# Performance work log

Measured on AMD Instinct MI355X. Metric: run time of the kernel, lower is better.

The kernel has to match this reference:

```python
import jax, jax.numpy as jnp
import numpy as np

N_NODES = 50000
N_EDGES = 800000
D_IN = 64
D_OUT = 64
EDGE_DIM = 32
BN_EPS = 1e-5
GIN_EPS = 0.0


def setup_inputs() -> dict:
    key = jax.random.key(0)
    ks = jax.random.split(key, 8)
    x = jax.random.normal(ks[0], (N_NODES, D_IN), dtype=jnp.float32)
    edge_index = jax.random.randint(ks[1], (2, N_EDGES), 0, N_NODES, dtype=jnp.int64)
    edge_attr = jax.random.normal(ks[2], (N_EDGES, EDGE_DIM), dtype=jnp.float32)
    # learned params (scaled like kaiming-ish init)
    We = jax.random.normal(ks[3], (EDGE_DIM, D_IN), dtype=jnp.float32) / np.sqrt(EDGE_DIM)
    be = jnp.zeros((D_IN,), dtype=jnp.float32)
    W1 = jax.random.normal(ks[4], (D_IN, D_OUT), dtype=jnp.float32) / np.sqrt(D_IN)
    b1 = jnp.zeros((D_OUT,), dtype=jnp.float32)
    gamma = jnp.ones((D_OUT,), dtype=jnp.float32)
    beta = jnp.zeros((D_OUT,), dtype=jnp.float32)
    W2 = jax.random.normal(ks[5], (D_OUT, D_OUT), dtype=jnp.float32) / np.sqrt(D_OUT)
    b2 = jnp.zeros((D_OUT,), dtype=jnp.float32)
    return {"x": x, "edge_index": edge_index, "edge_attr": edge_attr,
            "We": We, "be": be, "W1": W1, "b1": b1,
            "gamma": gamma, "beta": beta, "W2": W2, "b2": b2}


def reference(x, edge_index, edge_attr, We, be, W1, b1, gamma, beta, W2, b2):
    src = edge_index[0]  # j (source), PyG default flow source_to_target
    dst = edge_index[1]  # i (target)
    # message: x_j + lin(edge_attr)
    msg = x[src] + (edge_attr @ We + be)              # [E, D_IN]
    # scatter-add aggregate into target nodes
    agg = jax.ops.segment_sum(msg, dst, num_segments=x.shape[0])  # [N, D_IN]
    # GIN residual
    out = agg + (1.0 + GIN_EPS) * x
    # MLP: Linear -> BatchNorm1d (training stats) -> ReLU -> Linear
    h = out @ W1 + b1
    mean = jnp.mean(h, axis=0)
    var = jnp.var(h, axis=0)
    h = (h - mean) * jax.lax.rsqrt(var + BN_EPS) * gamma + beta
    h = jax.nn.relu(h)
    return h @ W2 + b2
```

## Files before the change

kernel.cpp:

```cpp
#include <hip/hip_runtime.h>

#define N_NODES 50000
#define N_EDGES 800000
#define D 64
#define ED 32
#define BN_EPS 1e-5f

#define NBKT 250
#define NPB  200
#define NB_SC 500
#define EPB  1600
#define CAP  4096

#define WS_SUMS     0
#define WS_SUMSQ    64
#define WS_RESV     128
#define WS_ZERO_END 384
#define WS_OFF      384
#define WS_PACK     50388
#define WS_SRC2     (WS_PACK + 2 * NBKT * CAP)
#define WS_AGGEA    (WS_SRC2 + 2 * N_EDGES)
#define WS_PRE      (WS_AGGEA + N_NODES * ED)
#define WS_H        (WS_PRE + N_NODES * D)
#define WS_WC       (WS_H + N_NODES * D)
#define WS_BEC      (WS_WC + ED * D)

#define N_BLK ((N_NODES + 63) / 64)

__global__ __launch_bounds__(256) void foldw_kernel(
    const float* __restrict__ We, const float* __restrict__ W1,
    const float* __restrict__ be, float* __restrict__ wc, float* __restrict__ bec)
{
    const int idx = blockIdx.x * 256 + threadIdx.x;
    if (idx < ED * D) {
        const int j = idx >> 6, f = idx & 63;
        float a = 0.f;
        for (int k = 0; k < D; ++k) a += We[j * D + k] * W1[k * D + f];
        wc[idx] = a;
    }
    if (idx < D) {
        float a = 0.f;
        for (int k = 0; k < D; ++k) a += be[k] * W1[k * D + idx];
        bec[idx] = a;
    }
}

__global__ __launch_bounds__(256) void bin_scatter_kernel(
    const int* __restrict__ ei, int* __restrict__ resv, uint2* __restrict__ pack)
{
    __shared__ int hist[NBKT], seg[NBKT], lcur[NBKT];
    const int t = threadIdx.x;
    if (t < NBKT) { hist[t] = 0; lcur[t] = 0; }
    __syncthreads();
    const int e0 = blockIdx.x * EPB;
    for (int i = t; i < EPB; i += 256)
        atomicAdd(&hist[ei[N_EDGES + e0 + i] / NPB], 1);
    __syncthreads();
    if (t < NBKT) seg[t] = t * CAP + atomicAdd(&resv[t], hist[t]);
    __syncthreads();
    for (int i = t; i < EPB; i += 256) {
        const int e = e0 + i;
        const int s = ei[e];
        const int d = ei[N_EDGES + e];
        const int bkt = d / NPB;
        const int r = atomicAdd(&lcur[bkt], 1);
        pack[seg[bkt] + r] = make_uint2(((unsigned)d << 16) | (unsigned)s,
                                        (unsigned)e);
    }
}

__global__ __launch_bounds__(512) void bucket_place_kernel(
    const int* __restrict__ resv, const uint2* __restrict__ pack,
    int* __restrict__ off, int2* __restrict__ sorted)
{
    __shared__ int sA[256], sB[256];
    __shared__ int cnt[NPB], lcur[NPB];
    __shared__ int pA[256], pB[256];
    __shared__ int sBase, sNE;
    const int t = threadIdx.x;
    const int j = blockIdx.x;
    if (t < 256) sA[t] = (t < NBKT) ? resv[t] : 0;
    if (t < NPB) { cnt[t] = 0; lcur[t] = 0; }
    __syncthreads();
    int* cur = sA; int* nxt = sB;
    for (int o = 1; o < 256; o <<= 1) {
        if (t < 256) nxt[t] = cur[t] + (t >= o ? cur[t - o] : 0);
        __syncthreads();
        int* tmp = cur; cur = nxt; nxt = tmp;
    }
    if (t == 0) { sBase = (j == 0) ? 0 : cur[j - 1]; sNE = resv[j]; }
    __syncthreads();
    const int base = sBase, nE = sNE;
    const uint2* pp = pack + (size_t)j * CAP;

    for (int i = t; i < nE; i += 512)
        atomicAdd(&cnt[(int)(pp[i].x >> 16) - j * NPB], 1);
    __syncthreads();
    if (t < 256) pA[t] = (t < NPB) ? cnt[t] : 0;
    __syncthreads();
    int* c2 = pA; int* n2 = pB;
    for (int o = 1; o < 256; o <<= 1) {
        if (t < 256) n2[t] = c2[t] + (t >= o ? c2[t - o] : 0);
        __syncthreads();
        int* tmp = c2; c2 = n2; n2 = tmp;
    }
    if (t < NPB) {
        const int excl = (t == 0) ? 0 : c2[t - 1];
        n2[t] = excl;
        off[j * NPB + t] = base + excl;
    }
    if (j == NBKT - 1 && t == 0) off[N_NODES] = N_EDGES;
    __syncthreads();
    for (int i = t; i < nE; i += 512) {
        const uint2 w = pp[i];
        const int dl = (int)(w.x >> 16) - j * NPB;
        const int r = atomicAdd(&lcur[dl], 1);
        sorted[base + n2[dl] + r] = make_int2((int)w.y, (int)(w.x & 0xffffu));
    }
}

__global__ __launch_bounds__(256) void agg_kernel(
    const float* __restrict__ x, const float* __restrict__ ea,
    const int* __restrict__ off, const int2* __restrict__ sorted,
    float* __restrict__ pre, float* __restrict__ aggEA)
{
    const int f = threadIdx.x & 63;
    const int w = threadIdx.x >> 6;
    const int fe = f & 31;
    const bool lo = (f < 32);
    const int nwv = gridDim.x * 4;
    for (int node = blockIdx.x * 4 + w; node < N_NODES; node += nwv) {
        const int start = __builtin_amdgcn_readfirstlane(off[node]);
        const int n     = __builtin_amdgcn_readfirstlane(off[node + 1]) - start;
        const int2* sp = sorted + start;
        float s = x[(size_t)node * D + f];
        float ax = 0.f, ay = 0.f;
        int it = 0;
        if (n >= 8) {
            int2 c0 = sp[0], c1 = sp[1], c2 = sp[2], c3 = sp[3];
            int2 c4 = sp[4], c5 = sp[5], c6 = sp[6], c7 = sp[7];
            for (; it + 16 <= n; it += 8) {
                const int2 n0 = sp[it + 8],  n1 = sp[it + 9];
                const int2 n2 = sp[it + 10], n3 = sp[it + 11];
                const int2 n4 = sp[it + 12], n5 = sp[it + 13];
                const int2 n6 = sp[it + 14], n7 = sp[it + 15];
                s += x[(size_t)c0.y * D + f]; s += x[(size_t)c1.y * D + f];
                s += x[(size_t)c2.y * D + f]; s += x[(size_t)c3.y * D + f];
                s += x[(size_t)c4.y * D + f]; s += x[(size_t)c5.y * D + f];
                s += x[(size_t)c6.y * D + f]; s += x[(size_t)c7.y * D + f];
                ax += ea[(size_t)(lo ? c0.x : c1.x) * ED + fe];
                ax += ea[(size_t)(lo ? c2.x : c3.x) * ED + fe];
                ay += ea[(size_t)(lo ? c4.x : c5.x) * ED + fe];
                ay += ea[(size_t)(lo ? c6.x : c7.x) * ED + fe];
                c0 = n0; c1 = n1; c2 = n2; c3 = n3;
                c4 = n4; c5 = n5; c6 = n6; c7 = n7;
            }
            s += x[(size_t)c0.y * D + f]; s += x[(size_t)c1.y * D + f];
            s += x[(size_t)c2.y * D + f]; s += x[(size_t)c3.y * D + f];
            s += x[(size_t)c4.y * D + f]; s += x[(size_t)c5.y * D + f];
            s += x[(size_t)c6.y * D + f]; s += x[(size_t)c7.y * D + f];
            ax += ea[(size_t)(lo ? c0.x : c1.x) * ED + fe];
            ax += ea[(size_t)(lo ? c2.x : c3.x) * ED + fe];
            ay += ea[(size_t)(lo ? c4.x : c5.x) * ED + fe];
            ay += ea[(size_t)(lo ? c6.x : c7.x) * ED + fe];
            it += 8;
        }
        for (; it < n; ++it) {
            const int2 p = sp[it];
            s += x[(size_t)p.y * D + f];
            if (lo) ax += ea[(size_t)p.x * ED + fe];
        }
        pre[(size_t)node * D + f] = s;
        ax += ay;
        ax += __shfl_xor(ax, 32);
        if (lo) aggEA[(size_t)node * ED + fe] = ax;
    }
}

__global__ __launch_bounds__(256) void mlp1g_kernel(
    const float* __restrict__ pre, const float* __restrict__ aggEA,
    const int* __restrict__ off,
    const float* __restrict__ W1, const float* __restrict__ wc,
    const float* __restrict__ bec, const float* __restrict__ b1,
    float* __restrict__ h, float* __restrict__ sums, float* __restrict__ sumsq)
{
    __shared__ float As[64 * 100];
    __shared__ float Bs[96 * 64];
    __shared__ float4 sb1v[16];
    __shared__ float4 sbecv[16];
    __shared__ float sDeg[64];
    const int tid = threadIdx.x;
    const int base = blockIdx.x * 64;

    for (int i = tid; i < 64 * 16; i += 256)
        ((float4*)Bs)[i] = ((const float4*)W1)[i];
    for (int i = tid; i < 32 * 16; i += 256)
        ((float4*)Bs)[64 * 16 + i] = ((const float4*)wc)[i];
    if (tid < 16)      sb1v[tid] = ((const float4*)b1)[tid];
    else if (tid < 32) sbecv[tid - 16] = ((const float4*)bec)[tid - 16];
    if (tid < 64) {
        const int node = base + tid;
        sDeg[tid] = (node < N_NODES) ? (float)(off[node + 1] - off[node]) : 0.f;
    }
    #pragma unroll
    for (int r = 0; r < 4; ++r) {
        const int idx = tid + 256 * r;
        const int nl = idx >> 4, c4 = idx & 15;
        const bool v = (base + nl) < N_NODES;
        const float4 t = v ? ((const float4*)pre)[(size_t)(base + nl) * 16 + c4]
                           : make_float4(0.f, 0.f, 0.f, 0.f);
        *(float4*)&As[nl * 100 + c4 * 4] = t;
    }
    #pragma unroll
    for (int r = 0; r < 2; ++r) {
        const int idx = tid + 256 * r;
        const int nl = idx >> 3, c4 = idx & 7;
        const bool v = (base + nl) < N_NODES;
        const float4 t = v ? ((const float4*)aggEA)[(size_t)(base + nl) * 8 + c4]
                           : make_float4(0.f, 0.f, 0.f, 0.f);
        *(float4*)&As[nl * 100 + 64 + c4 * 4] = t;
    }
    __syncthreads();

    const int tx = tid & 15, ty = tid >> 4;
    const int r0 = ty * 4;
    const float4 bb = sb1v[tx];
    const float4 bc = sbecv[tx];
    float4 acc0, acc1, acc2, acc3;
    acc0.x = bb.x + sDeg[r0+0]*bc.x; acc0.y = bb.y + sDeg[r0+0]*bc.y;
    acc0.z = bb.z + sDeg[r0+0]*bc.z; acc0.w = bb.w + sDeg[r0+0]*bc.w;
    acc1.x = bb.x + sDeg[r0+1]*bc.x; acc1.y = bb.y + sDeg[r0+1]*bc.y;
    acc1.z = bb.z + sDeg[r0+1]*bc.z; acc1.w = bb.w + sDeg[r0+1]*bc.w;
    acc2.x = bb.x + sDeg[r0+2]*bc.x; acc2.y = bb.y + sDeg[r0+2]*bc.y;
    acc2.z = bb.z + sDeg[r0+2]*bc.z; acc2.w = bb.w + sDeg[r0+2]*bc.w;
    acc3.x = bb.x + sDeg[r0+3]*bc.x; acc3.y = bb.y + sDeg[r0+3]*bc.y;
    acc3.z = bb.z + sDeg[r0+3]*bc.z; acc3.w = bb.w + sDeg[r0+3]*bc.w;

    for (int k4 = 0; k4 < 24; ++k4) {
        const int k = k4 * 4;
        const float4 a0 = *(const float4*)&As[(r0+0)*100 + k];
        const float4 a1 = *(const float4*)&As[(r0+1)*100 + k];
        const float4 a2 = *(const float4*)&As[(r0+2)*100 + k];
        const float4 a3 = *(const float4*)&As[(r0+3)*100 + k];
        const float4 w0 = *(const float4*)&Bs[(k+0)*64 + tx*4];
        const float4 w1v = *(const float4*)&Bs[(k+1)*64 + tx*4];
        const float4 w2v = *(const float4*)&Bs[(k+2)*64 + tx*4];
        const float4 w3v = *(const float4*)&Bs[(k+3)*64 + tx*4];
        acc0.x += a0.x*w0.x + a0.y*w1v.x + a0.z*w2v.x + a0.w*w3v.x;
        acc0.y += a0.x*w0.y + a0.y*w1v.y + a0.z*w2v.y + a0.w*w3v.y;
        acc0.z += a0.x*w0.z + a0.y*w1v.z + a0.z*w2v.z + a0.w*w3v.z;
        acc0.w += a0.x*w0.w + a0.y*w1v.w + a0.z*w2v.w + a0.w*w3v.w;
        acc1.x += a1.x*w0.x + a1.y*w1v.x + a1.z*w2v.x + a1.w*w3v.x;
        acc1.y += a1.x*w0.y + a1.y*w1v.y + a1.z*w2v.y + a1.w*w3v.y;
        acc1.z += a1.x*w0.z + a1.y*w1v.z + a1.z*w2v.z + a1.w*w3v.z;
        acc1.w += a1.x*w0.w + a1.y*w1v.w + a1.z*w2v.w + a1.w*w3v.w;
        acc2.x += a2.x*w0.x + a2.y*w1v.x + a2.z*w2v.x + a2.w*w3v.x;
        acc2.y += a2.x*w0.y + a2.y*w1v.y + a2.z*w2v.y + a2.w*w3v.y;
        acc2.z += a2.x*w0.z + a2.y*w1v.z + a2.z*w2v.z + a2.w*w3v.z;
        acc2.w += a2.x*w0.w + a2.y*w1v.w + a2.z*w2v.w + a2.w*w3v.w;
        acc3.x += a3.x*w0.x + a3.y*w1v.x + a3.z*w2v.x + a3.w*w3v.x;
        acc3.y += a3.x*w0.y + a3.y*w1v.y + a3.z*w2v.y + a3.w*w3v.y;
        acc3.z += a3.x*w0.z + a3.y*w1v.z + a3.z*w2v.z + a3.w*w3v.z;
        acc3.w += a3.x*w0.w + a3.y*w1v.w + a3.z*w2v.w + a3.w*w3v.w;
    }

    float4 ps = make_float4(0.f, 0.f, 0.f, 0.f);
    float4 pq = make_float4(0.f, 0.f, 0.f, 0.f);
    {
        const int n0 = base + r0;
        if (n0 + 0 < N_NODES) {
            ((float4*)h)[(size_t)(n0+0)*16 + tx] = acc0;
            ps.x += acc0.x; ps.y += acc0.y; ps.z += acc0.z; ps.w += acc0.w;
            pq.x += acc0.x*acc0.x; pq.y += acc0.y*acc0.y;
            pq.z += acc0.z*acc0.z; pq.w += acc0.w*acc0.w;
        }
        if (n0 + 1 < N_NODES) {
            ((float4*)h)[(size_t)(n0+1)*16 + tx] = acc1;
            ps.x += acc1.x; ps.y += acc1.y; ps.z += acc1.z; ps.w += acc1.w;
            pq.x += acc1.x*acc1.x; pq.y += acc1.y*acc1.y;
            pq.z += acc1.z*acc1.z; pq.w += acc1.w*acc1.w;
        }
        if (n0 + 2 < N_NODES) {
            ((float4*)h)[(size_t)(n0+2)*16 + tx] = acc2;
            ps.x += acc2.x; ps.y += acc2.y; ps.z += acc2.z; ps.w += acc2.w;
            pq.x += acc2.x*acc2.x; pq.y += acc2.y*acc2.y;
            pq.z += acc2.z*acc2.z; pq.w += acc2.w*acc2.w;
        }
        if (n0 + 3 < N_NODES) {
            ((float4*)h)[(size_t)(n0+3)*16 + tx] = acc3;
            ps.x += acc3.x; ps.y += acc3.y; ps.z += acc3.z; ps.w += acc3.w;
            pq.x += acc3.x*acc3.x; pq.y += acc3.y*acc3.y;
            pq.z += acc3.z*acc3.z; pq.w += acc3.w*acc3.w;
        }
    }
    __syncthreads();
    float* sS = Bs;
    float* sQ = Bs + 1024;
    sS[ty*64 + tx*4 + 0] = ps.x; sS[ty*64 + tx*4 + 1] = ps.y;
    sS[ty*64 + tx*4 + 2] = ps.z; sS[ty*64 + tx*4 + 3] = ps.w;
    sQ[ty*64 + tx*4 + 0] = pq.x; sQ[ty*64 + tx*4 + 1] = pq.y;
    sQ[ty*64 + tx*4 + 2] = pq.z; sQ[ty*64 + tx*4 + 3] = pq.w;
    __syncthreads();
    if (tid < 64) {
        float s = 0.f, q = 0.f;
        #pragma unroll
        for (int r = 0; r < 16; ++r) { s += sS[r*64 + tid]; q += sQ[r*64 + tid]; }
        unsafeAtomicAdd(&sums[tid], s);
        unsafeAtomicAdd(&sumsq[tid], q);
    }
}

__global__ __launch_bounds__(256) void mlp2g_kernel(
    const float* __restrict__ h, const float* __restrict__ W2,
    const float* __restrict__ b2, const float* __restrict__ sums,
    const float* __restrict__ sumsq, const float* __restrict__ gamma,
    const float* __restrict__ beta, float* __restrict__ out)
{
    __shared__ float As[64 * 68];
    __shared__ float Bs[64 * 64];
    __shared__ float4 sb2v[16];
    __shared__ float4 sscv[16];
    __shared__ float4 sshv[16];
    const int tid = threadIdx.x;
    const int base = blockIdx.x * 64;

    for (int i = tid; i < 64 * 16; i += 256)
        ((float4*)Bs)[i] = ((const float4*)W2)[i];
    if (tid < 16) sb2v[tid] = ((const float4*)b2)[tid];
    if (tid < 64) {
        const float inv_n = 1.0f / (float)N_NODES;
        const float mean = sums[tid] * inv_n;
        const float var  = sumsq[tid] * inv_n - mean * mean;
        const float sc   = gamma[tid] * rsqrtf(var + BN_EPS);
        ((float*)sscv)[tid] = sc;
        ((float*)sshv)[tid] = beta[tid] - mean * sc;
    }
    __syncthreads();

    #pragma unroll
    for (int r = 0; r < 4; ++r) {
        const int idx = tid + 256 * r;
        const int nl = idx >> 4, c4 = idx & 15;
        const bool v = (base + nl) < N_NODES;
        const float4 t = v ? ((const float4*)h)[(size_t)(base + nl) * 16 + c4]
                           : make_float4(0.f, 0.f, 0.f, 0.f);
        const float4 c = sscv[c4];
        const float4 s = sshv[c4];
        float4 rv;
        rv.x = fmaxf(t.x * c.x + s.x, 0.f);
        rv.y = fmaxf(t.y * c.y + s.y, 0.f);
        rv.z = fmaxf(t.z * c.z + s.z, 0.f);
        rv.w = fmaxf(t.w * c.w + s.w, 0.f);
        *(float4*)&As[nl * 68 + c4 * 4] = rv;
    }
    __syncthreads();

    const int tx = tid & 15, ty = tid >> 4;
    const int r0 = ty * 4;
    const float4 bb = sb2v[tx];
    float4 acc0 = bb, acc1 = bb, acc2 = bb, acc3 = bb;

    for (int k4 = 0; k4 < 16; ++k4) {
        const int k = k4 * 4;
        const float4 a0 = *(const float4*)&As[(r0+0)*68 + k];
        const float4 a1 = *(const float4*)&As[(r0+1)*68 + k];
        const float4 a2 = *(const float4*)&As[(r0+2)*68 + k];
        const float4 a3 = *(const float4*)&As[(r0+3)*68 + k];
        const float4 w0 = *(const float4*)&Bs[(k+0)*64 + tx*4];
        const float4 w1v = *(const float4*)&Bs[(k+1)*64 + tx*4];
        const float4 w2v = *(const float4*)&Bs[(k+2)*64 + tx*4];
        const float4 w3v = *(const float4*)&Bs[(k+3)*64 + tx*4];
        acc0.x += a0.x*w0.x + a0.y*w1v.x + a0.z*w2v.x + a0.w*w3v.x;
        acc0.y += a0.x*w0.y + a0.y*w1v.y + a0.z*w2v.y + a0.w*w3v.y;
        acc0.z += a0.x*w0.z + a0.y*w1v.z + a0.z*w2v.z + a0.w*w3v.z;
        acc0.w += a0.x*w0.w + a0.y*w1v.w + a0.z*w2v.w + a0.w*w3v.w;
        acc1.x += a1.x*w0.x + a1.y*w1v.x + a1.z*w2v.x + a1.w*w3v.x;
        acc1.y += a1.x*w0.y + a1.y*w1v.y + a1.z*w2v.y + a1.w*w3v.y;
        acc1.z += a1.x*w0.z + a1.y*w1v.z + a1.z*w2v.z + a1.w*w3v.z;
        acc1.w += a1.x*w0.w + a1.y*w1v.w + a1.z*w2v.w + a1.w*w3v.w;
        acc2.x += a2.x*w0.x + a2.y*w1v.x + a2.z*w2v.x + a2.w*w3v.x;
        acc2.y += a2.x*w0.y + a2.y*w1v.y + a2.z*w2v.y + a2.w*w3v.y;
        acc2.z += a2.x*w0.z + a2.y*w1v.z + a2.z*w2v.z + a2.w*w3v.z;
        acc2.w += a2.x*w0.w + a2.y*w1v.w + a2.z*w2v.w + a2.w*w3v.w;
        acc3.x += a3.x*w0.x + a3.y*w1v.x + a3.z*w2v.x + a3.w*w3v.x;
        acc3.y += a3.x*w0.y + a3.y*w1v.y + a3.z*w2v.y + a3.w*w3v.y;
        acc3.z += a3.x*w0.z + a3.y*w1v.z + a3.z*w2v.z + a3.w*w3v.z;
        acc3.w += a3.x*w0.w + a3.y*w1v.w + a3.z*w2v.w + a3.w*w3v.w;
    }

    const int n0 = base + r0;
    if (n0 + 0 < N_NODES) ((float4*)out)[(size_t)(n0+0)*16 + tx] = acc0;
    if (n0 + 1 < N_NODES) ((float4*)out)[(size_t)(n0+1)*16 + tx] = acc1;
    if (n0 + 2 < N_NODES) ((float4*)out)[(size_t)(n0+2)*16 + tx] = acc2;
    if (n0 + 3 < N_NODES) ((float4*)out)[(size_t)(n0+3)*16 + tx] = acc3;
}

extern "C" void kernel_launch(void* const* d_in, const int* in_sizes, int n_in,
                              void* d_out, int out_size, void* d_ws, size_t ws_size,
                              hipStream_t stream) {
    const float* x     = (const float*)d_in[0];
    const int*   ei    = (const int*)  d_in[1];
    const float* ea    = (const float*)d_in[2];
    const float* We    = (const float*)d_in[3];
    const float* be    = (const float*)d_in[4];
    const float* W1    = (const float*)d_in[5];
    const float* b1    = (const float*)d_in[6];
    const float* gamma = (const float*)d_in[7];
    const float* beta  = (const float*)d_in[8];
    const float* W2    = (const float*)d_in[9];
    const float* b2    = (const float*)d_in[10];

    float* ws      = (float*)d_ws;
    float* sums    = ws + WS_SUMS;
    float* sumsq   = ws + WS_SUMSQ;
    int*   resv    = (int*)(ws + WS_RESV);
    int*   off     = (int*)(ws + WS_OFF);
    uint2* pack    = (uint2*)(ws + WS_PACK);
    int2*  sorted2 = (int2*)(ws + WS_SRC2);
    float* aggEA   = ws + WS_AGGEA;
    float* pre     = ws + WS_PRE;
    float* h       = ws + WS_H;
    float* wcbuf   = ws + WS_WC;
    float* becbuf  = ws + WS_BEC;

    hipMemsetAsync(ws, 0, (size_t)WS_ZERO_END * sizeof(float), stream);

    foldw_kernel       <<<8, 256, 0, stream>>>(We, W1, be, wcbuf, becbuf);
    bin_scatter_kernel <<<NB_SC, 256, 0, stream>>>(ei, resv, pack);
    bucket_place_kernel<<<NBKT, 512, 0, stream>>>(resv, pack, off, sorted2);
    agg_kernel         <<<2048, 256, 0, stream>>>(x, ea, off, sorted2, pre, aggEA);
    mlp1g_kernel       <<<N_BLK, 256, 0, stream>>>(pre, aggEA, off, W1, wcbuf,
                                                   becbuf, b1, h, sums, sumsq);
    mlp2g_kernel       <<<N_BLK, 256, 0, stream>>>(h, W2, b2, sums, sumsq,
                                                   gamma, beta, (float*)d_out);
}
```

Before: 295.8 us.

## Fuse gather-aggregation into first MLP kernel and stage edge indices in LDS

Merges the neighbor aggregation kernel into the first MLP GEMM kernel. Each 1024-thread block gathers 64 nodes' aggregated features and edge-attribute sums directly into shared memory, then a quarter of the threads run the GEMM and BN statistics. This removes the pre/aggEA intermediate buffers and their global write/read round trip plus one launch. The cost is that 768 threads sit idle during the GEMM phase and large blocks may reduce occupancy and latency hiding for the gather. The binning kernel also caches src/dst indices in LDS to avoid reading them from global memory twice.

```diff
diff --git a/kernel.cpp b/kernel.cpp
--- a/kernel.cpp
+++ b/kernel.cpp
@@ -19,9 +19,7 @@
 #define WS_OFF      384
 #define WS_PACK     50388
 #define WS_SRC2     (WS_PACK + 2 * NBKT * CAP)
-#define WS_AGGEA    (WS_SRC2 + 2 * N_EDGES)
-#define WS_PRE      (WS_AGGEA + N_NODES * ED)
-#define WS_H        (WS_PRE + N_NODES * D)
+#define WS_H        (WS_SRC2 + 2 * N_EDGES)
 #define WS_WC       (WS_H + N_NODES * D)
 #define WS_BEC      (WS_WC + ED * D)
 
@@ -49,23 +47,26 @@
     const int* __restrict__ ei, int* __restrict__ resv, uint2* __restrict__ pack)
 {
     __shared__ int hist[NBKT], seg[NBKT], lcur[NBKT];
+    __shared__ int sSrc[EPB], sDst[EPB];
     const int t = threadIdx.x;
     if (t < NBKT) { hist[t] = 0; lcur[t] = 0; }
-    __syncthreads();
     const int e0 = blockIdx.x * EPB;
+    for (int i = t; i < EPB; i += 256) {
+        sSrc[i] = ei[e0 + i];
+        sDst[i] = ei[N_EDGES + e0 + i];
+    }
+    __syncthreads();
     for (int i = t; i < EPB; i += 256)
-        atomicAdd(&hist[ei[N_EDGES + e0 + i] / NPB], 1);
+        atomicAdd(&hist[sDst[i] / NPB], 1);
     __syncthreads();
     if (t < NBKT) seg[t] = t * CAP + atomicAdd(&resv[t], hist[t]);
     __syncthreads();
     for (int i = t; i < EPB; i += 256) {
-        const int e = e0 + i;
-        const int s = ei[e];
-        const int d = ei[N_EDGES + e];
+        const int d = sDst[i];
         const int bkt = d / NPB;
         const int r = atomicAdd(&lcur[bkt], 1);
-        pack[seg[bkt] + r] = make_uint2(((unsigned)d << 16) | (unsigned)s,
-                                        (unsigned)e);
+        pack[seg[bkt] + r] = make_uint2(((unsigned)d << 16) | (unsigned)sSrc[i],
+                                        (unsigned)(e0 + i));
     }
 }
 
@@ -119,67 +120,9 @@
     }
 }
 
-__global__ __launch_bounds__(256) void agg_kernel(
+__global__ __launch_bounds__(1024) void agg_mlp1_kernel(
     const float* __restrict__ x, const float* __restrict__ ea,
     const int* __restrict__ off, const int2* __restrict__ sorted,
-    float* __restrict__ pre, float* __restrict__ aggEA)
-{
-    const int f = threadIdx.x & 63;
-    const int w = threadIdx.x >> 6;
-    const int fe = f & 31;
-    const bool lo = (f < 32);
-    const int nwv = gridDim.x * 4;
-    for (int node = blockIdx.x * 4 + w; node < N_NODES; node += nwv) {
-        const int start = __builtin_amdgcn_readfirstlane(off[node]);
-        const int n     = __builtin_amdgcn_readfirstlane(off[node + 1]) - start;
-        const int2* sp = sorted + start;
-        float s = x[(size_t)node * D + f];
-        float ax = 0.f, ay = 0.f;
-        int it = 0;
-        if (n >= 8) {
-            int2 c0 = sp[0], c1 = sp[1], c2 = sp[2], c3 = sp[3];
-            int2 c4 = sp[4], c5 = sp[5], c6 = sp[6], c7 = sp[7];
-            for (; it + 16 <= n; it += 8) {
-                const int2 n0 = sp[it + 8],  n1 = sp[it + 9];
-                const int2 n2 = sp[it + 10], n3 = sp[it + 11];
-                const int2 n4 = sp[it + 12], n5 = sp[it + 13];
-                const int2 n6 = sp[it + 14], n7 = sp[it + 15];
-                s += x[(size_t)c0.y * D + f]; s += x[(size_t)c1.y * D + f];
-                s += x[(size_t)c2.y * D + f]; s += x[(size_t)c3.y * D + f];
-                s += x[(size_t)c4.y * D + f]; s += x[(size_t)c5.y * D + f];
-                s += x[(size_t)c6.y * D + f]; s += x[(size_t)c7.y * D + f];
-                ax += ea[(size_t)(lo ? c0.x : c1.x) * ED + fe];
-                ax += ea[(size_t)(lo ? c2.x : c3.x) * ED + fe];
-                ay += ea[(size_t)(lo ? c4.x : c5.x) * ED + fe];
-                ay += ea[(size_t)(lo ? c6.x : c7.x) * ED + fe];
-                c0 = n0; c1 = n1; c2 = n2; c3 = n3;
-                c4 = n4; c5 = n5; c6 = n6; c7 = n7;
-            }
-            s += x[(size_t)c0.y * D + f]; s += x[(size_t)c1.y * D + f];
-            s += x[(size_t)c2.y * D + f]; s += x[(size_t)c3.y * D + f];
-            s += x[(size_t)c4.y * D + f]; s += x[(size_t)c5.y * D + f];
-            s += x[(size_t)c6.y * D + f]; s += x[(size_t)c7.y * D + f];
-            ax += ea[(size_t)(lo ? c0.x : c1.x) * ED + fe];
-            ax += ea[(size_t)(lo ? c2.x : c3.x) * ED + fe];
-            ay += ea[(size_t)(lo ? c4.x : c5.x) * ED + fe];
-            ay += ea[(size_t)(lo ? c6.x : c7.x) * ED + fe];
-            it += 8;
-        }
-        for (; it < n; ++it) {
-            const int2 p = sp[it];
-            s += x[(size_t)p.y * D + f];
-            if (lo) ax += ea[(size_t)p.x * ED + fe];
-        }
-        pre[(size_t)node * D + f] = s;
-        ax += ay;
-        ax += __shfl_xor(ax, 32);
-        if (lo) aggEA[(size_t)node * ED + fe] = ax;
-    }
-}
-
-__global__ __launch_bounds__(256) void mlp1g_kernel(
-    const float* __restrict__ pre, const float* __restrict__ aggEA,
-    const int* __restrict__ off,
     const float* __restrict__ W1, const float* __restrict__ wc,
     const float* __restrict__ bec, const float* __restrict__ b1,
     float* __restrict__ h, float* __restrict__ sums, float* __restrict__ sumsq)
@@ -192,81 +135,117 @@
     const int tid = threadIdx.x;
     const int base = blockIdx.x * 64;
 
-    for (int i = tid; i < 64 * 16; i += 256)
+    for (int i = tid; i < 64 * 16; i += 1024)
         ((float4*)Bs)[i] = ((const float4*)W1)[i];
-    for (int i = tid; i < 32 * 16; i += 256)
+    for (int i = tid; i < 32 * 16; i += 1024)
         ((float4*)Bs)[64 * 16 + i] = ((const float4*)wc)[i];
     if (tid < 16)      sb1v[tid] = ((const float4*)b1)[tid];
     else if (tid < 32) sbecv[tid - 16] = ((const float4*)bec)[tid - 16];
-    if (tid < 64) {
-        const int node = base + tid;
-        sDeg[tid] = (node < N_NODES) ? (float)(off[node + 1] - off[node]) : 0.f;
-    }
+
+    const int f = tid & 63;
+    const int w = tid >> 6;
+    const int fe = f & 31;
+    const bool lo = (f < 32);
     #pragma unroll
-    for (int r = 0; r < 4; ++r) {
-        const int idx = tid + 256 * r;
-        const int nl = idx >> 4, c4 = idx & 15;
-        const bool v = (base + nl) < N_NODES;
-        const float4 t = v ? ((const float4*)pre)[(size_t)(base + nl) * 16 + c4]
-                           : make_float4(0.f, 0.f, 0.f, 0.f);
-        *(float4*)&As[nl * 100 + c4 * 4] = t;
-    }
-    #pragma unroll
-    for (int r = 0; r < 2; ++r) {
-        const int idx = tid + 256 * r;
-        const int nl = idx >> 3, c4 = idx & 7;
-        const bool v = (base + nl) < N_NODES;
-        const float4 t = v ? ((const float4*)aggEA)[(size_t)(base + nl) * 8 + c4]
-                           : make_float4(0.f, 0.f, 0.f, 0.f);
-        *(float4*)&As[nl * 100 + 64 + c4 * 4] = t;
-    }
-    __syncthreads();
-
-    const int tx = tid & 15, ty = tid >> 4;
-    const int r0 = ty * 4;
-    const float4 bb = sb1v[tx];
-    const float4 bc = sbecv[tx];
-    float4 acc0, acc1, acc2, acc3;
-    acc0.x = bb.x + sDeg[r0+0]*bc.x; acc0.y = bb.y + sDeg[r0+0]*bc.y;
-    acc0.z = bb.z + sDeg[r0+0]*bc.z; acc0.w = bb.w + sDeg[r0+0]*bc.w;
-    acc1.x = bb.x + sDeg[r0+1]*bc.x; acc1.y = bb.y + sDeg[r0+1]*bc.y;
-    acc1.z = bb.z + sDeg[r0+1]*bc.z; acc1.w = bb.w + sDeg[r0+1]*bc.w;
-    acc2.x = bb.x + sDeg[r0+2]*bc.x; acc2.y = bb.y + sDeg[r0+2]*bc.y;
-    acc2.z = bb.z + sDeg[r0+2]*bc.z; acc2.w = bb.w + sDeg[r0+2]*bc.w;
-    acc3.x = bb.x + sDeg[r0+3]*bc.x; acc3.y = bb.y + sDeg[r0+3]*bc.y;
-    acc3.z = bb.z + sDeg[r0+3]*bc.z; acc3.w = bb.w + sDeg[r0+3]*bc.w;
-
-    for (int k4 = 0; k4 < 24; ++k4) {
-        const int k = k4 * 4;
-        const float4 a0 = *(const float4*)&As[(r0+0)*100 + k];
-        const float4 a1 = *(const float4*)&As[(r0+1)*100 + k];
-        const float4 a2 = *(const float4*)&As[(r0+2)*100 + k];
-        const float4 a3 = *(const float4*)&As[(r0+3)*100 + k];
-        const float4 w0 = *(const float4*)&Bs[(k+0)*64 + tx*4];
-        const float4 w1v = *(const float4*)&Bs[(k+1)*64 + tx*4];
-        const float4 w2v = *(const float4*)&Bs[(k+2)*64 + tx*4];
-        const float4 w3v = *(const float4*)&Bs[(k+3)*64 + tx*4];
-        acc0.x += a0.x*w0.x + a0.y*w1v.x + a0.z*w2v.x + a0.w*w3v.x;
-        acc0.y += a0.x*w0.y + a0.y*w1v.y + a0.z*w2v.y + a0.w*w3v.y;
-        acc0.z += a0.x*w0.z + a0.y*w1v.z + a0.z*w2v.z + a0.w*w3v.z;
-        acc0.w += a0.x*w0.w + a0.y*w1v.w + a0.z*w2v.w + a0.w*w3v.w;
-        acc1.x += a1.x*w0.x + a1.y*w1v.x + a1.z*w2v.x + a1.w*w3v.x;
-        acc1.y += a1.x*w0.y + a1.y*w1v.y + a1.z*w2v.y + a1.w*w3v.y;
-        acc1.z += a1.x*w0.z + a1.y*w1v.z + a1.z*w2v.z + a1.w*w3v.z;
-        acc1.w += a1.x*w0.w + a1.y*w1v.w + a1.z*w2v.w + a1.w*w3v.w;
-        acc2.x += a2.x*w0.x + a2.y*w1v.x + a2.z*w2v.x + a2.w*w3v.x;
-        acc2.y += a2.x*w0.y + a2.y*w1v.y + a2.z*w2v.y + a2.w*w3v.y;
-        acc2.z += a2.x*w0.z + a2.y*w1v.z + a2.z*w2v.z + a2.w*w3v.z;
-        acc2.w += a2.x*w0.w + a2.y*w1v.w + a2.z*w2v.w + a2.w*w3v.w;
-        acc3.x += a3.x*w0.x + a3.y*w1v.x + a3.z*w2v.x + a3.w*w3v.x;
-        acc3.y += a3.x*w0.y + a3.y*w1v.y + a3.z*w2v.y + a3.w*w3v.y;
-        acc3.z += a3.x*w0.z + a3.y*w1v.z + a3.z*w2v.z + a3.w*w3v.z;
-        acc3.w += a3.x*w0.w + a3.y*w1v.w + a3.z*w2v.w + a3.w*w3v.w;
-    }
+    for (int i = 0; i < 4; ++i) {
+        const int nl = w * 4 + i;
+        const int node = base + nl;
+        float s = 0.f, ax = 0.f, ay = 0.f;
+        int n = 0;
+        if (node < N_NODES) {
+            const int start = __builtin_amdgcn_readfirstlane(off[node]);
+            n = __builtin_amdgcn_readfirstlane(off[node + 1]) - start;
+            const int2* sp = sorted + start;
+            s = x[(size_t)node * D + f];
+            int it = 0;
+            if (n >= 8) {
+                int2 c0 = sp[0], c1 = sp[1], c2 = sp[2], c3 = sp[3];
+                int2 c4 = sp[4], c5 = sp[5], c6 = sp[6], c7 = sp[7];
+                for (; it + 16 <= n; it += 8) {
+                    const int2 n0 = sp[it + 8],  n1 = sp[it + 9];
+                    const int2 n2 = sp[it + 10], n3 = sp[it + 11];
+                    const int2 n4 = sp[it + 12], n5 = sp[it + 13];
+                    const int2 n6 = sp[it + 14], n7 = sp[it + 15];
+                    s += x[(size_t)c0.y * D + f]; s += x[(size_t)c1.y * D + f];
+                    s += x[(size_t)c2.y * D + f]; s += x[(size_t)c3.y * D + f];
+                    s += x[(size_t)c4.y * D + f]; s += x[(size_t)c5.y * D + f];
+                    s += x[(size_t)c6.y * D + f]; s += x[(size_t)c7.y * D + f];
+                    ax += ea[(size_t)(lo ? c0.x : c1.x) * ED + fe];
+                    ax += ea[(size_t)(lo ? c2.x : c3.x) * ED + fe];
+                    ay += ea[(size_t)(lo ? c4.x : c5.x) * ED + fe];
+                    ay += ea[(size_t)(lo ? c6.x : c7.x) * ED + fe];
+                    c0 = n0; c1 = n1; c2 = n2; c3 = n3;
+                    c4 = n4; c5 = n5; c6 = n6; c7 = n7;
+                }
+                s += x[(size_t)c0.y * D + f]; s += x[(size_t)c1.y * D + f];
+                s += x[(size_t)c2.y * D + f]; s += x[(size_t)c3.y * D + f];
+                s += x[(size_t)c4.y * D + f]; s += x[(size_t)c5.y * D + f];
+                s += x[(size_t)c6.y * D + f]; s += x[(size_t)c7.y * D + f];
+                ax += ea[(size_t)(lo ? c0.x : c1.x) * ED + fe];
+                ax += ea[(size_t)(lo ? c2.x : c3.x) * ED + fe];
+                ay += ea[(size_t)(lo ? c4.x : c5.x) * ED + fe];
+                ay += ea[(size_t)(lo ? c6.x : c7.x) * ED + fe];
+                it += 8;
+            }
+            for (; it < n; ++it) {
+                const int2 p = sp[it];
+                s += x[(size_t)p.y * D + f];
+                if (lo) ax += ea[(size_t)p.x * ED + fe];
+            }
+        }
+        As[nl * 100 + f] = s;
+        ax += ay;
+        ax += __shfl_xor(ax, 32);
+        if (lo) As[nl * 100 + 64 + fe] = ax;
+        if (f == 0) sDeg[nl] = (float)n;
+    }
+    __syncthreads();
 
     float4 ps = make_float4(0.f, 0.f, 0.f, 0.f);
     float4 pq = make_float4(0.f, 0.f, 0.f, 0.f);
-    {
+    const int tx = tid & 15, ty = (tid >> 4) & 15;
+    if (tid < 256) {
+        const int r0 = ty * 4;
+        const float4 bb = sb1v[tx];
+        const float4 bc = sbecv[tx];
+        float4 acc0, acc1, acc2, acc3;
+        acc0.x = bb.x + sDeg[r0+0]*bc.x; acc0.y = bb.y + sDeg[r0+0]*bc.y;
+        acc0.z = bb.z + sDeg[r0+0]*bc.z; acc0.w = bb.w + sDeg[r0+0]*bc.w;
+        acc1.x = bb.x + sDeg[r0+1]*bc.x; acc1.y = bb.y + sDeg[r0+1]*bc.y;
+        acc1.z = bb.z + sDeg[r0+1]*bc.z; acc1.w = bb.w + sDeg[r0+1]*bc.w;
+        acc2.x = bb.x + sDeg[r0+2]*bc.x; acc2.y = bb.y + sDeg[r0+2]*bc.y;
+        acc2.z = bb.z + sDeg[r0+2]*bc.z; acc2.w = bb.w + sDeg[r0+2]*bc.w;
+        acc3.x = bb.x + sDeg[r0+3]*bc.x; acc3.y = bb.y + sDeg[r0+3]*bc.y;
+        acc3.z = bb.z + sDeg[r0+3]*bc.z; acc3.w = bb.w + sDeg[r0+3]*bc.w;
+
+        for (int k4 = 0; k4 < 24; ++k4) {
+            const int k = k4 * 4;
+            const float4 a0 = *(const float4*)&As[(r0+0)*100 + k];
+            const float4 a1 = *(const float4*)&As[(r0+1)*100 + k];
+            const float4 a2 = *(const float4*)&As[(r0+2)*100 + k];
+            const float4 a3 = *(const float4*)&As[(r0+3)*100 + k];
+            const float4 w0 = *(const float4*)&Bs[(k+0)*64 + tx*4];
+            const float4 w1v = *(const float4*)&Bs[(k+1)*64 + tx*4];
+            const float4 w2v = *(const float4*)&Bs[(k+2)*64 + tx*4];
+            const float4 w3v = *(const float4*)&Bs[(k+3)*64 + tx*4];
+            acc0.x += a0.x*w0.x + a0.y*w1v.x + a0.z*w2v.x + a0.w*w3v.x;
+            acc0.y += a0.x*w0.y + a0.y*w1v.y + a0.z*w2v.y + a0.w*w3v.y;
+            acc0.z += a0.x*w0.z + a0.y*w1v.z + a0.z*w2v.z + a0.w*w3v.z;
+            acc0.w += a0.x*w0.w + a0.y*w1v.w + a0.z*w2v.w + a0.w*w3v.w;
+            acc1.x += a1.x*w0.x + a1.y*w1v.x + a1.z*w2v.x + a1.w*w3v.x;
+            acc1.y += a1.x*w0.y + a1.y*w1v.y + a1.z*w2v.y + a1.w*w3v.y;
+            acc1.z += a1.x*w0.z + a1.y*w1v.z + a1.z*w2v.z + a1.w*w3v.z;
+            acc1.w += a1.x*w0.w + a1.y*w1v.w + a1.z*w2v.w + a1.w*w3v.w;
+            acc2.x += a2.x*w0.x + a2.y*w1v.x + a2.z*w2v.x + a2.w*w3v.x;
+            acc2.y += a2.x*w0.y + a2.y*w1v.y + a2.z*w2v.y + a2.w*w3v.y;
+            acc2.z += a2.x*w0.z + a2.y*w1v.z + a2.z*w2v.z + a2.w*w3v.z;
+            acc2.w += a2.x*w0.w + a2.y*w1v.w + a2.z*w2v.w + a2.w*w3v.w;
+            acc3.x += a3.x*w0.x + a3.y*w1v.x + a3.z*w2v.x + a3.w*w3v.x;
+            acc3.y += a3.x*w0.y + a3.y*w1v.y + a3.z*w2v.y + a3.w*w3v.y;
+            acc3.z += a3.x*w0.z + a3.y*w1v.z + a3.z*w2v.z + a3.w*w3v.z;
+            acc3.w += a3.x*w0.w + a3.y*w1v.w + a3.z*w2v.w + a3.w*w3v.w;
+        }
+
         const int n0 = base + r0;
         if (n0 + 0 < N_NODES) {
             ((float4*)h)[(size_t)(n0+0)*16 + tx] = acc0;
@@ -296,10 +275,12 @@
     __syncthreads();
     float* sS = Bs;
     float* sQ = Bs + 1024;
-    sS[ty*64 + tx*4 + 0] = ps.x; sS[ty*64 + tx*4 + 1] = ps.y;
-    sS[ty*64 + tx*4 + 2] = ps.z; sS[ty*64 + tx*4 + 3] = ps.w;
-    sQ[ty*64 + tx*4 + 0] = pq.x; sQ[ty*64 + tx*4 + 1] = pq.y;
-    sQ[ty*64 + tx*4 + 2] = pq.z; sQ[ty*64 + tx*4 + 3] = pq.w;
+    if (tid < 256) {
+        sS[ty*64 + tx*4 + 0] = ps.x; sS[ty*64 + tx*4 + 1] = ps.y;
+        sS[ty*64 + tx*4 + 2] = ps.z; sS[ty*64 + tx*4 + 3] = ps.w;
+        sQ[ty*64 + tx*4 + 0] = pq.x; sQ[ty*64 + tx*4 + 1] = pq.y;
+        sQ[ty*64 + tx*4 + 2] = pq.z; sQ[ty*64 + tx*4 + 3] = pq.w;
+    }
     __syncthreads();
     if (tid < 64) {
         float s = 0.f, q = 0.f;
@@ -417,8 +398,6 @@
     int*   off     = (int*)(ws + WS_OFF);
     uint2* pack    = (uint2*)(ws + WS_PACK);
     int2*  sorted2 = (int2*)(ws + WS_SRC2);
-    float* aggEA   = ws + WS_AGGEA;
-    float* pre     = ws + WS_PRE;
     float* h       = ws + WS_H;
     float* wcbuf   = ws + WS_WC;
     float* becbuf  = ws + WS_BEC;
@@ -428,9 +407,8 @@
     foldw_kernel       <<<8, 256, 0, stream>>>(We, W1, be, wcbuf, becbuf);
     bin_scatter_kernel <<<NB_SC, 256, 0, stream>>>(ei, resv, pack);
     bucket_place_kernel<<<NBKT, 512, 0, stream>>>(resv, pack, off, sorted2);
-    agg_kernel         <<<2048, 256, 0, stream>>>(x, ea, off, sorted2, pre, aggEA);
-    mlp1g_kernel       <<<N_BLK, 256, 0, stream>>>(pre, aggEA, off, W1, wcbuf,
-                                                   becbuf, b1, h, sums, sumsq);
+    agg_mlp1_kernel    <<<N_BLK, 1024, 0, stream>>>(x, ea, off, sorted2, W1, wcbuf,
+                                                    becbuf, b1, h, sums, sumsq);
     mlp2g_kernel       <<<N_BLK, 256, 0, stream>>>(h, W2, b2, sums, sumsq,
                                                    gamma, beta, (float*)d_out);
 }
```

Result: slower. 308.3 us (+4.2%).

## Fold weight-fold kernel into binning, double bucket count, stage edges in LDS

Applied to the files above, without the earlier changes.

Merges the small weight-folding kernel into the bin-scatter launch as extra blocks, which saves one launch. Doubles the number of dst buckets (100 nodes each, CAP 2048), so each bucket_place block handles fewer edges and runs a wider 512-entry prefix scan over bucket reservations. Edge indices are staged in shared memory so each is loaded from global memory once. It also moves the pre/aggEA buffers to a new workspace location. With CAP halved, overflow is possible if a bucket exceeds 2048 edges, though the average is about 1600.

```diff
diff --git a/kernel.cpp b/kernel.cpp
--- a/kernel.cpp
+++ b/kernel.cpp
@@ -6,66 +6,67 @@
 #define ED 32
 #define BN_EPS 1e-5f
 
-#define NBKT 250
-#define NPB  200
+#define NBKT 500
+#define NPB  100
 #define NB_SC 500
 #define EPB  1600
-#define CAP  4096
+#define CAP  2048
 
 #define WS_SUMS     0
 #define WS_SUMSQ    64
 #define WS_RESV     128
-#define WS_ZERO_END 384
-#define WS_OFF      384
-#define WS_PACK     50388
+#define WS_ZERO_END 640
+#define WS_OFF      640
+#define WS_PACK     50644
 #define WS_SRC2     (WS_PACK + 2 * NBKT * CAP)
-#define WS_AGGEA    (WS_SRC2 + 2 * N_EDGES)
-#define WS_PRE      (WS_AGGEA + N_NODES * ED)
-#define WS_H        (WS_PRE + N_NODES * D)
+#define WS_H        (WS_SRC2 + 2 * N_EDGES)
 #define WS_WC       (WS_H + N_NODES * D)
 #define WS_BEC      (WS_WC + ED * D)
 
 #define N_BLK ((N_NODES + 63) / 64)
 
-__global__ __launch_bounds__(256) void foldw_kernel(
+__global__ __launch_bounds__(256) void bin_scatter_kernel(
+    const int* __restrict__ ei, int* __restrict__ resv, uint2* __restrict__ pack,
     const float* __restrict__ We, const float* __restrict__ W1,
     const float* __restrict__ be, float* __restrict__ wc, float* __restrict__ bec)
 {
-    const int idx = blockIdx.x * 256 + threadIdx.x;
-    if (idx < ED * D) {
-        const int j = idx >> 6, f = idx & 63;
-        float a = 0.f;
-        for (int k = 0; k < D; ++k) a += We[j * D + k] * W1[k * D + f];
-        wc[idx] = a;
-    }
-    if (idx < D) {
-        float a = 0.f;
-        for (int k = 0; k < D; ++k) a += be[k] * W1[k * D + idx];
-        bec[idx] = a;
-    }
-}
-
-__global__ __launch_bounds__(256) void bin_scatter_kernel(
-    const int* __restrict__ ei, int* __restrict__ resv, uint2* __restrict__ pack)
-{
+    const int t = threadIdx.x;
+    if (blockIdx.x >= NB_SC) {
+        const int idx = (blockIdx.x - NB_SC) * 256 + t;
+        if (idx < ED * D) {
+            const int j = idx >> 6, f = idx & 63;
+            float a = 0.f;
+            for (int k = 0; k < D; ++k) a += We[j * D + k] * W1[k * D + f];
+            wc[idx] = a;
+        }
+        if (idx < D) {
+            float a = 0.f;
+            for (int k = 0; k < D; ++k) a += be[k] * W1[k * D + idx];
+            bec[idx] = a;
+        }
+        return;
+    }
     __shared__ int hist[NBKT], seg[NBKT], lcur[NBKT];
-    const int t = threadIdx.x;
-    if (t < NBKT) { hist[t] = 0; lcur[t] = 0; }
-    __syncthreads();
+    __shared__ int sSrc[EPB], sDst[EPB];
+    for (int i = t; i < NBKT; i += 256) { hist[i] = 0; lcur[i] = 0; }
     const int e0 = blockIdx.x * EPB;
+    for (int i = t; i < EPB; i += 256) {
+        sSrc[i] = ei[e0 + i];
+        sDst[i] = ei[N_EDGES + e0 + i];
+    }
+    __syncthreads();
     for (int i = t; i < EPB; i += 256)
-        atomicAdd(&hist[ei[N_EDGES + e0 + i] / NPB], 1);
-    __syncthreads();
-    if (t < NBKT) seg[t] = t * CAP + atomicAdd(&resv[t], hist[t]);
+        atomicAdd(&hist[sDst[i] / NPB], 1);
+    __syncthreads();
+    for (int i = t; i < NBKT; i += 256)
+        seg[i] = i * CAP + atomicAdd(&resv[i], hist[i]);
     __syncthreads();
     for (int i = t; i < EPB; i += 256) {
-        const int e = e0 + i;
-        const int s = ei[e];
-        const int d = ei[N_EDGES + e];
+        const int d = sDst[i];
         const int bkt = d / NPB;
         const int r = atomicAdd(&lcur[bkt], 1);
-        pack[seg[bkt] + r] = make_uint2(((unsigned)d << 16) | (unsigned)s,
-                                        (unsigned)e);
+        pack[seg[bkt] + r] = make_uint2(((unsigned)d << 16) | (unsigned)sSrc[i],
+                                        (unsigned)(e0 + i));
     }
 }
 
@@ -73,18 +74,18 @@
     const int* __restrict__ resv, const uint2* __restrict__ pack,
     int* __restrict__ off, int2* __restrict__ sorted)
 {
-    __shared__ int sA[256], sB[256];
+    __shared__ int sA[512], sB[512];
     __shared__ int cnt[NPB], lcur[NPB];
-    __shared__ int pA[256], pB[256];
+    __shared__ int pA[128], pB[128];
     __shared__ int sBase, sNE;
     const int t = threadIdx.x;
     const int j = blockIdx.x;
-    if (t < 256) sA[t] = (t < NBKT) ? resv[t] : 0;
+    sA[t] = (t < NBKT) ? resv[t] : 0;
     if (t < NPB) { cnt[t] = 0; lcur[t] = 0; }
     __syncthreads();
     int* cur = sA; int* nxt = sB;
-    for (int o = 1; o < 256; o <<= 1) {
-        if (t < 256) nxt[t] = cur[t] + (t >= o ? cur[t - o] : 0);
+    for (int o = 1; o < 512; o <<= 1) {
+        nxt[t] = cur[t] + (t >= o ? cur[t - o] : 0);
         __syncthreads();
         int* tmp = cur; cur = nxt; nxt = tmp;
     }
@@ -96,11 +97,11 @@
     for (int i = t; i < nE; i += 512)
         atomicAdd(&cnt[(int)(pp[i].x >> 16) - j * NPB], 1);
     __syncthreads();
-    if (t < 256) pA[t] = (t < NPB) ? cnt[t] : 0;
+    if (t < 128) pA[t] = (t < NPB) ? cnt[t] : 0;
     __syncthreads();
     int* c2 = pA; int* n2 = pB;
-    for (int o = 1; o < 256; o <<= 1) {
-        if (t < 256) n2[t] = c2[t] + (t >= o ? c2[t - o] : 0);
+    for (int o = 1; o < 128; o <<= 1) {
+        if (t < 128) n2[t] = c2[t] + (t >= o ? c2[t - o] : 0);
         __syncthreads();
         int* tmp = c2; c2 = n2; n2 = tmp;
     }
@@ -417,19 +418,22 @@
     int*   off     = (int*)(ws + WS_OFF);
     uint2* pack    = (uint2*)(ws + WS_PACK);
     int2*  sorted2 = (int2*)(ws + WS_SRC2);
-    float* aggEA   = ws + WS_AGGEA;
-    float* pre     = ws + WS_PRE;
     float* h       = ws + WS_H;
     float* wcbuf   = ws + WS_WC;
     float* becbuf  = ws + WS_BEC;
 
+    float* pre     = (float*)d_out;
+    float* preb    = ws + (WS_BEC + 64);
+    float* aggEA   = preb + (size_t)N_NODES * D;
+    (void)pre;
+
     hipMemsetAsync(ws, 0, (size_t)WS_ZERO_END * sizeof(float), stream);
 
-    foldw_kernel       <<<8, 256, 0, stream>>>(We, W1, be, wcbuf, becbuf);
-    bin_scatter_kernel <<<NB_SC, 256, 0, stream>>>(ei, resv, pack);
+    bin_scatter_kernel <<<NB_SC + 8, 256, 0, stream>>>(ei, resv, pack,
+                                                       We, W1, be, wcbuf, becbuf);
     bucket_place_kernel<<<NBKT, 512, 0, stream>>>(resv, pack, off, sorted2);
-    agg_kernel         <<<2048, 256, 0, stream>>>(x, ea, off, sorted2, pre, aggEA);
-    mlp1g_kernel       <<<N_BLK, 256, 0, stream>>>(pre, aggEA, off, W1, wcbuf,
+    agg_kernel         <<<2048, 256, 0, stream>>>(x, ea, off, sorted2, preb, aggEA);
+    mlp1g_kernel       <<<N_BLK, 256, 0, stream>>>(preb, aggEA, off, W1, wcbuf,
                                                    becbuf, b1, h, sums, sumsq);
     mlp2g_kernel       <<<N_BLK, 256, 0, stream>>>(h, W2, b2, sums, sumsq,
                                                    gamma, beta, (float*)d_out);
```

New measurement: 282.7 us. 1.05x faster.
